# Optimization experiments

Hardware: AMD Instinct MI355X
Metric: run time of the kernel (lower is better)

## Reference

```python
import jax, jax.numpy as jnp
import numpy as np

B, C, L = 32, 64, 512
PATCH_LEN = 16
PATCH_NUM = L // PATCH_LEN
H = 512          # hidden_dim
FF = 512         # moe_d_ff == hidden_dim per __init__
E = 8            # num_experts
TOP_K = 2


def setup_inputs() -> dict:
    key = jax.random.key(0)
    ks = jax.random.split(key, 8)
    s = 0.02
    return {
        "x": jax.random.normal(ks[0], (B, C, L), dtype=jnp.float32),
        "Wp": jax.random.normal(ks[1], (H, PATCH_LEN), dtype=jnp.float32) * s,
        "bp": jnp.zeros((H,), dtype=jnp.float32),
        "Wg": jax.random.normal(ks[2], (E, H), dtype=jnp.float32) * s,
        "Wgate": jax.random.normal(ks[3], (E, FF, H), dtype=jnp.float32) * s,
        "Wup": jax.random.normal(ks[4], (E, FF, H), dtype=jnp.float32) * s,
        "Wdown": jax.random.normal(ks[5], (E, H, FF), dtype=jnp.float32) * s,
    }


def reference(x, Wp, bp, Wg, Wgate, Wup, Wdown):
    b, c, l = x.shape
    # patchify: [B, C, P, patch_len] -> project to hidden
    p = x.reshape(b, c, PATCH_NUM, PATCH_LEN)
    h = jnp.einsum("bcpl,dl->bcpd", p, Wp) + bp          # [B,C,P,H]
    tokens = h.reshape(-1, H)                               # [T,H]
    T = tokens.shape[0]

    # router: softmax in fp32, then top-k (norm_topk_prob=False)
    logits = tokens @ Wg.T                                   # [T,E]
    rw = jax.nn.softmax(logits.astype(jnp.float32), axis=-1)
    topw, topi = jax.lax.top_k(rw, TOP_K)                    # [T,K]

    # dense per-(token,expert) combine weight, equiv. to gather/scatter combine
    w = jnp.zeros((T, E), dtype=jnp.float32)
    w = w.at[jnp.arange(T)[:, None], topi].add(topw)         # [T,E]

    out = jnp.zeros((T, H), dtype=tokens.dtype)
    for e in range(E):  # fixed small expert loop
        g = jax.nn.silu(tokens @ Wgate[e].T)
        u = tokens @ Wup[e].T
        y = (g * u) @ Wdown[e].T                             # [T,H]
        out = out + (w[:, e:e + 1] * y.astype(jnp.float32)).astype(tokens.dtype)

    return out.reshape(b, c * PATCH_NUM, H)
```

## Files before the change

kernel.cpp:

```cpp
#include <hip/hip_runtime.h>
#include <hip/hip_bf16.h>
#include <cstdint>
#include <cstddef>

typedef __attribute__((ext_vector_type(8))) short short8;
typedef __attribute__((ext_vector_type(4))) float f32x4;

#define GLL16(g, l) __builtin_amdgcn_global_load_lds(                         \
    (const __attribute__((address_space(1))) void*)(g),                        \
    (__attribute__((address_space(3))) void*)(l), 16, 0, 0)

constexpr int kB = 32, kC = 64, kL = 512;
constexpr int kPL = 16, kPN = 32;
constexpr int kH = 512, kFF = 512, kE = 8;
constexpr int kT = kB * kC * kPN;
constexpr int kTilesPerSlot = 520;
constexpr int kMaxTiles = 2 * kTilesPerSlot;
constexpr int kMaxPairs = kMaxTiles * 128;

constexpr size_t OFF_TOK  = 0;
constexpr size_t OFF_GU   = OFF_TOK + (size_t)kT * kH * 2;
constexpr size_t OFF_TOPI = OFF_GU + (size_t)kMaxPairs * kFF * 2;
constexpr size_t OFF_TOPW = OFF_TOPI + (size_t)kT * 4;
constexpr size_t OFF_CCNT = OFF_TOPW + (size_t)kT * 8;
constexpr size_t OFF_COFF = OFF_CCNT + 256 * 16 * 4;
constexpr size_t OFF_EOFF = OFF_COFF + 256 * 16 * 4;
constexpr size_t OFF_TILE = OFF_EOFF + 256;
constexpr size_t OFF_PTOK = OFF_TILE + ((kMaxTiles * 4 + 255) & ~255ull);
constexpr size_t OFF_PW   = OFF_PTOK + (size_t)kMaxPairs * 4;
constexpr size_t OFF_DUMP = OFF_PW + (size_t)kMaxPairs * 4;
constexpr size_t OFF_BG   = OFF_DUMP + 128 * 512 * 4;
constexpr size_t OFF_BU   = OFF_BG + (size_t)kE * kFF * kH * 2;
constexpr size_t OFF_BD   = OFF_BU + (size_t)kE * kFF * kH * 2;
constexpr size_t OFF_WC   = OFF_BD + (size_t)kE * kH * kFF * 2;
constexpr size_t OFF_BC   = OFF_WC + 8 * 16 * 8;

__global__ __launch_bounds__(256) void k_conv3(const float* __restrict__ a,
                                               const float* __restrict__ b,
                                               const float* __restrict__ c,
                                               __hip_bfloat16* __restrict__ da,
                                               __hip_bfloat16* __restrict__ db,
                                               __hip_bfloat16* __restrict__ dc, int n) {
  for (int i = blockIdx.x * blockDim.x + threadIdx.x; i < 3 * n; i += gridDim.x * blockDim.x) {
    int reg = i / n, j = i - reg * n;
    const float* s = (reg == 0) ? a : (reg == 1) ? b : c;
    __hip_bfloat16* d = (reg == 0) ? da : (reg == 1) ? db : dc;
    d[j] = __float2bfloat16(s[j]);
  }
}

__global__ void k_wcomb(const float* __restrict__ Wg, const float* __restrict__ Wp,
                        const float* __restrict__ bp, double* __restrict__ wc,
                        double* __restrict__ bc) {
  int tid = threadIdx.x;
  int e = tid >> 4, l = tid & 15;
  double s = 0.0;
  for (int d = 0; d < kH; ++d) s += (double)Wg[e * kH + d] * (double)Wp[d * kPL + l];
  wc[e * kPL + l] = s;
  if (l == 0) {
    double b = 0.0;
    for (int d = 0; d < kH; ++d) b += (double)Wg[e * kH + d] * (double)bp[d];
    bc[e] = b;
  }
}

__global__ __launch_bounds__(256) void k_patch(const float* __restrict__ x,
                                               const float* __restrict__ Wp,
                                               const float* __restrict__ bp,
                                               __hip_bfloat16* __restrict__ tok) {
  __shared__ float sWp[512 * 17];
  __shared__ float sx[128];
  __shared__ float sbp[512];
  int bb = blockIdx.x;
  int bc = bb >> 2, pg = bb & 3;
  int tid = threadIdx.x;
  for (int i = tid; i < 512 * 16; i += 256) sWp[(i >> 4) * 17 + (i & 15)] = Wp[i];
  if (tid < 128) sx[tid] = x[(size_t)bc * 512 + pg * 128 + tid];
  for (int i = tid; i < 512; i += 256) sbp[i] = bp[i];
  __syncthreads();
  for (int tl = 0; tl < 8; ++tl) {
    int t = bc * kPN + pg * 8 + tl;
    const float* xp = &sx[tl * 16];
    for (int d = tid; d < 512; d += 256) {
      float s = sbp[d];
#pragma unroll
      for (int l = 0; l < 16; ++l) s += xp[l] * sWp[d * 17 + l];
      tok[(size_t)t * kH + d] = __float2bfloat16(s);
    }
  }
}

__global__ __launch_bounds__(256) void k_router(const float* __restrict__ x,
                                                const double* __restrict__ wc,
                                                const double* __restrict__ bc,
                                                int* __restrict__ topi,
                                                float* __restrict__ topw,
                                                int* __restrict__ chunkCnt) {
  int t = blockIdx.x * 256 + threadIdx.x;
  int bci = t >> 5, p = t & 31;
  const float* xp = &x[(size_t)bci * 512 + p * 16];
  double xl[16];
#pragma unroll
  for (int l = 0; l < 16; ++l) xl[l] = (double)xp[l];
  double lo[8];
  double m = -1e300;
#pragma unroll
  for (int e = 0; e < 8; ++e) {
    double s = bc[e];
#pragma unroll
    for (int l = 0; l < 16; ++l) s += xl[l] * wc[e * 16 + l];
    lo[e] = s;
    m = fmax(m, s);
  }
  double den = 0.0;
#pragma unroll
  for (int e = 0; e < 8; ++e) {
    lo[e] = exp(lo[e] - m);
    den += lo[e];
  }
  int i1 = 0;
  double v1 = lo[0];
#pragma unroll
  for (int e = 1; e < 8; ++e)
    if (lo[e] > v1) { v1 = lo[e]; i1 = e; }
  int i2 = -1;
  double v2 = -1.0;
#pragma unroll
  for (int e = 0; e < 8; ++e)
    if (e != i1 && lo[e] > v2) { v2 = lo[e]; i2 = e; }
  topi[t] = i1 | (i2 << 4);
  topw[2 * t] = (float)(v1 / den);
  topw[2 * t + 1] = (float)(v2 / den);

  __shared__ int wsum[16][4];
  int wave = threadIdx.x >> 6, lane = threadIdx.x & 63;
#pragma unroll
  for (int seg = 0; seg < 16; ++seg) {
    int e = seg & 7;
    bool sel = (seg < 8) ? (i1 == e) : (i2 == e);
    unsigned long long mm = __ballot(sel);
    if (lane == 0) wsum[seg][wave] = __popcll(mm);
  }
  __syncthreads();
  if (threadIdx.x < 16)
    chunkCnt[blockIdx.x * 16 + threadIdx.x] =
        wsum[threadIdx.x][0] + wsum[threadIdx.x][1] + wsum[threadIdx.x][2] + wsum[threadIdx.x][3];
}

__global__ __launch_bounds__(256) void k_scan(const int* __restrict__ chunkCnt,
                                              int* __restrict__ chunkOff,
                                              int* __restrict__ eoff,
                                              int* __restrict__ tileExpert,
                                              int* __restrict__ pairTok,
                                              float* __restrict__ pairW) {
  int tid = threadIdx.x;
  __shared__ int totals[16];
  __shared__ int base[16];
  __shared__ int padded[16];
  if (tid < 16) {
    int run = 0;
    for (int c = 0; c < 256; ++c) {
      chunkOff[c * 16 + tid] = run;
      run += chunkCnt[c * 16 + tid];
    }
    totals[tid] = run;
  }
  __syncthreads();
  if (tid == 0) {
    for (int s = 0; s < 2; ++s) {
      int b = s * kTilesPerSlot * 128;
      for (int e = 0; e < 8; ++e) {
        int seg = s * 8 + e;
        base[seg] = b;
        padded[seg] = (totals[seg] + 127) & ~127;
        b += padded[seg];
      }
    }
  }
  __syncthreads();
  if (tid < 16) eoff[tid] = base[tid];
  for (int tI = tid; tI < kMaxTiles; tI += 256) tileExpert[tI] = -1;
  __syncthreads();
  for (int seg = 0; seg < 16; ++seg) {
    int e = seg & 7;
    int tile0 = base[seg] >> 7, nt = padded[seg] >> 7;
    for (int tI = tid; tI < nt; tI += 256) tileExpert[tile0 + tI] = e;
    for (int p = base[seg] + totals[seg] + tid; p < base[seg] + padded[seg]; p += 256) {
      pairTok[p] = -1;
      pairW[p] = 0.f;
    }
  }
}

__global__ __launch_bounds__(256) void k_fill(const int* __restrict__ topi,
                                              const float* __restrict__ topw,
                                              const int* __restrict__ chunkOff,
                                              const int* __restrict__ eoff,
                                              int* __restrict__ pairTok,
                                              float* __restrict__ pairW) {
  int chunk = blockIdx.x;
  int t = chunk * 256 + threadIdx.x;
  int pk = topi[t];
  int i1 = pk & 15, i2 = (pk >> 4) & 15;
  float w1 = topw[2 * t], w2 = topw[2 * t + 1];
  int wave = threadIdx.x >> 6, lane = threadIdx.x & 63;
  __shared__ int wsum[16][4];
  int pre[16];
  bool sel[16];
#pragma unroll
  for (int seg = 0; seg < 16; ++seg) {
    int e = seg & 7;
    sel[seg] = (seg < 8) ? (i1 == e) : (i2 == e);
    unsigned long long mm = __ballot(sel[seg]);
    pre[seg] = __popcll(mm & ((1ull << lane) - 1));
    if (lane == 0) wsum[seg][wave] = __popcll(mm);
  }
  __syncthreads();
#pragma unroll
  for (int seg = 0; seg < 16; ++seg) {
    if (!sel[seg]) continue;
    int woff = 0;
    for (int w = 0; w < wave; ++w) woff += wsum[seg][w];
    int pos = eoff[seg] + chunkOff[chunk * 16 + seg] + woff + pre[seg];
    pairTok[pos] = t;
    pairW[pos] = (seg < 8) ? w1 : w2;
  }
}


__global__ __launch_bounds__(256, 2) void k_gateup_sp(const __hip_bfloat16* __restrict__ tok,
                                                      const __hip_bfloat16* __restrict__ Wg0,
                                                      const __hip_bfloat16* __restrict__ Wu0,
                                                      const int* __restrict__ pairTok,
                                                      const int* __restrict__ tileExpert,
                                                      __hip_bfloat16* __restrict__ GU) {
  const int e = tileExpert[blockIdx.x];
  if (e < 0) return;
  __shared__ __hip_bfloat16 As[128 * 32];
  __shared__ __hip_bfloat16 Bgs[128 * 32];
  __shared__ __hip_bfloat16 Bus[128 * 32];
  const int tid = threadIdx.x;
  const int wid = tid >> 6, lane = tid & 63;
  const int tileBase = blockIdx.x * 128, tileN = blockIdx.y * 128;
  const int wr = wid >> 1, wcol = wid & 1;
  const int r = lane & 15, kq = lane >> 4;

  f32x4 accg[4][4] = {};
  f32x4 accu[4][4] = {};

  const char* Ab = (const char*)tok;
  const char* Bgb = (const char*)(Wg0 + (size_t)e * kFF * kH);
  const char* Bub = (const char*)(Wu0 + (size_t)e * kFF * kH);
  const int off0 = wid * 1024 + lane * 16;
  const int row0 = off0 >> 6;
  const int col0 = ((((off0 >> 4) & 3) ^ ((row0 >> 1) & 3)) << 4);
  const int off1 = off0 + 4096;
  const int row1 = off1 >> 6;
  const int col1 = ((((off1 >> 4) & 3) ^ ((row1 >> 1) & 3)) << 4);
  int t0i = pairTok[tileBase + row0];
  int t1i = pairTok[tileBase + row1];
  const size_t t0 = (size_t)(t0i < 0 ? 0 : t0i);
  const size_t t1 = (size_t)(t1i < 0 ? 0 : t1i);

#pragma unroll 1
  for (int kt = 0; kt < 16; ++kt) {
    const int kb = kt * 64;
    GLL16(Ab + t0 * 1024 + kb + col0, (char*)As + wid * 1024);
    GLL16(Ab + t1 * 1024 + kb + col1, (char*)As + 4096 + wid * 1024);
    GLL16(Bgb + (size_t)(tileN + row0) * 1024 + kb + col0, (char*)Bgs + wid * 1024);
    GLL16(Bgb + (size_t)(tileN + row1) * 1024 + kb + col1, (char*)Bgs + 4096 + wid * 1024);
    GLL16(Bub + (size_t)(tileN + row0) * 1024 + kb + col0, (char*)Bus + wid * 1024);
    GLL16(Bub + (size_t)(tileN + row1) * 1024 + kb + col1, (char*)Bus + 4096 + wid * 1024);
    __syncthreads();

    short8 a[4], bg[4], bu[4];
#pragma unroll
    for (int i = 0; i < 4; ++i) {
      int row = wr * 64 + i * 16 + r;
      int sc = (kq ^ ((row >> 1) & 3)) << 3;
      a[i] = *(const short8*)&As[row * 32 + sc];
    }
#pragma unroll
    for (int j = 0; j < 4; ++j) {
      int row = wcol * 64 + j * 16 + r;
      int sc = (kq ^ ((row >> 1) & 3)) << 3;
      bg[j] = *(const short8*)&Bgs[row * 32 + sc];
      bu[j] = *(const short8*)&Bus[row * 32 + sc];
    }
#pragma unroll
    for (int i = 0; i < 4; ++i)
#pragma unroll
      for (int j = 0; j < 4; ++j) {
        accg[i][j] = __builtin_amdgcn_mfma_f32_16x16x32_bf16(a[i], bg[j], accg[i][j], 0, 0, 0);
        accu[i][j] = __builtin_amdgcn_mfma_f32_16x16x32_bf16(a[i], bu[j], accu[i][j], 0, 0, 0);
      }
    __syncthreads();
  }

#pragma unroll
  for (int i = 0; i < 4; ++i)
#pragma unroll
    for (int j = 0; j < 4; ++j)
#pragma unroll
      for (int q = 0; q < 4; ++q) {
        int row = tileBase + wr * 64 + i * 16 + kq * 4 + q;
        int col = tileN + wcol * 64 + j * 16 + r;
        float g = accg[i][j][q], u = accu[i][j][q];
        float val = g / (1.f + __expf(-g)) * u;
        GU[(size_t)row * kFF + col] = __float2bfloat16(val);
      }
}

__global__ __launch_bounds__(256, 2) void k_down_sp(const __hip_bfloat16* __restrict__ GU,
                                                    const __hip_bfloat16* __restrict__ Wd0,
                                                    const int* __restrict__ pairTok,
                                                    const float* __restrict__ pairW,
                                                    const int* __restrict__ tileExpert,
                                                    float* __restrict__ out,
                                                    float* __restrict__ dump,
                                                    int tileOff, int first) {
  const int tile = tileOff + blockIdx.x;
  const int e = tileExpert[tile];
  if (e < 0) return;
  __shared__ __hip_bfloat16 As[128 * 32];
  __shared__ __hip_bfloat16 Bs[128 * 32];
  const int tid = threadIdx.x;
  const int wid = tid >> 6, lane = tid & 63;
  const int tileBase = tile * 128, tileN = blockIdx.y * 128;
  const int wr = wid >> 1, wcol = wid & 1;
  const int r = lane & 15, kq = lane >> 4;

  f32x4 acc[4][4] = {};

  const char* Ab = (const char*)GU;
  const char* Bb = (const char*)(Wd0 + (size_t)e * kH * kFF);
  const int off0 = wid * 1024 + lane * 16;
  const int row0 = off0 >> 6;
  const int col0 = ((((off0 >> 4) & 3) ^ ((row0 >> 1) & 3)) << 4);
  const int off1 = off0 + 4096;
  const int row1 = off1 >> 6;
  const int col1 = ((((off1 >> 4) & 3) ^ ((row1 >> 1) & 3)) << 4);

#pragma unroll 1
  for (int kt = 0; kt < 16; ++kt) {
    const int kb = kt * 64;
    GLL16(Ab + (size_t)(tileBase + row0) * 1024 + kb + col0, (char*)As + wid * 1024);
    GLL16(Ab + (size_t)(tileBase + row1) * 1024 + kb + col1, (char*)As + 4096 + wid * 1024);
    GLL16(Bb + (size_t)(tileN + row0) * 1024 + kb + col0, (char*)Bs + wid * 1024);
    GLL16(Bb + (size_t)(tileN + row1) * 1024 + kb + col1, (char*)Bs + 4096 + wid * 1024);
    __syncthreads();

    short8 a[4], b[4];
#pragma unroll
    for (int i = 0; i < 4; ++i) {
      int row = wr * 64 + i * 16 + r;
      int sc = (kq ^ ((row >> 1) & 3)) << 3;
      a[i] = *(const short8*)&As[row * 32 + sc];
    }
#pragma unroll
    for (int j = 0; j < 4; ++j) {
      int row = wcol * 64 + j * 16 + r;
      int sc = (kq ^ ((row >> 1) & 3)) << 3;
      b[j] = *(const short8*)&Bs[row * 32 + sc];
    }
#pragma unroll
    for (int i = 0; i < 4; ++i)
#pragma unroll
      for (int j = 0; j < 4; ++j)
        acc[i][j] = __builtin_amdgcn_mfma_f32_16x16x32_bf16(a[i], b[j], acc[i][j], 0, 0, 0);
    __syncthreads();
  }

#pragma unroll
  for (int i = 0; i < 4; ++i)
#pragma unroll
    for (int q = 0; q < 4; ++q) {
      int prow = tileBase + wr * 64 + i * 16 + kq * 4 + q;
      float wv = pairW[prow];
      int tk = pairTok[prow];
      int colBase = tileN + wcol * 64 + r;
      float* orow = (tk >= 0) ? out + (size_t)tk * kH + colBase
                              : dump + (size_t)(prow & 127) * kH + colBase;
#pragma unroll
      for (int j = 0; j < 4; ++j) {
        float val = acc[i][j][q] * wv;
        if (first) orow[j * 16] = val;
        else orow[j * 16] += val;
      }
    }
}

extern "C" void kernel_launch(void* const* d_in, const int* in_sizes, int n_in,
                              void* d_out, int out_size, void* d_ws, size_t ws_size,
                              hipStream_t stream) {
  const float* x = (const float*)d_in[0];
  const float* Wp = (const float*)d_in[1];
  const float* bp = (const float*)d_in[2];
  const float* Wg = (const float*)d_in[3];
  const float* Wgate = (const float*)d_in[4];
  const float* Wup = (const float*)d_in[5];
  const float* Wdown = (const float*)d_in[6];
  float* out = (float*)d_out;

  char* ws = (char*)d_ws;
  __hip_bfloat16* tok = (__hip_bfloat16*)(ws + OFF_TOK);
  __hip_bfloat16* gu = (__hip_bfloat16*)(ws + OFF_GU);
  int* topi = (int*)(ws + OFF_TOPI);
  float* topw = (float*)(ws + OFF_TOPW);
  int* chunkCnt = (int*)(ws + OFF_CCNT);
  int* chunkOff = (int*)(ws + OFF_COFF);
  int* eoff = (int*)(ws + OFF_EOFF);
  int* tileExpert = (int*)(ws + OFF_TILE);
  int* pairTok = (int*)(ws + OFF_PTOK);
  float* pairW = (float*)(ws + OFF_PW);
  float* dump = (float*)(ws + OFF_DUMP);
  __hip_bfloat16* bgw = (__hip_bfloat16*)(ws + OFF_BG);
  __hip_bfloat16* buw = (__hip_bfloat16*)(ws + OFF_BU);
  __hip_bfloat16* bdw = (__hip_bfloat16*)(ws + OFF_BD);
  double* wc = (double*)(ws + OFF_WC);
  double* bcv = (double*)(ws + OFF_BC);

  const int nw = kE * kFF * kH;
  k_conv3<<<3072, 256, 0, stream>>>(Wgate, Wup, Wdown, bgw, buw, bdw, nw);
  k_wcomb<<<1, 128, 0, stream>>>(Wg, Wp, bp, wc, bcv);
  k_patch<<<8192, 256, 0, stream>>>(x, Wp, bp, tok);
  k_router<<<256, 256, 0, stream>>>(x, wc, bcv, topi, topw, chunkCnt);
  k_scan<<<1, 256, 0, stream>>>(chunkCnt, chunkOff, eoff, tileExpert, pairTok, pairW);
  k_fill<<<256, 256, 0, stream>>>(topi, topw, chunkOff, eoff, pairTok, pairW);

  dim3 gg(kMaxTiles, 4);
  k_gateup_sp<<<gg, 256, 0, stream>>>(tok, bgw, buw, pairTok, tileExpert, gu);
  dim3 gd(kTilesPerSlot, 4);
  k_down_sp<<<gd, 256, 0, stream>>>(gu, bdw, pairTok, pairW, tileExpert, out, dump, 0, 1);
  k_down_sp<<<gd, 256, 0, stream>>>(gu, bdw, pairTok, pairW, tileExpert, out, dump,
                                    kTilesPerSlot, 0);
}
```

Baseline: 542.3 us.

## Double-buffer LDS tiles in gate/up and down GEMMs; scan chunk counts in LDS

The gate/up and down expert GEMM kernels now use two LDS buffers. The next K-slice is issued with global_load_lds before the MFMAs on the current slice run, and the barrier at the end of each iteration waits for the prefetched data. This is meant to hide global load latency behind compute, at the cost of twice the LDS per block, which may lower occupancy. Separately, k_scan stages chunk counts and offsets in shared memory, so the serial per-segment prefix loop no longer reads and writes global memory directly.

```diff
diff --git a/kernel.cpp b/kernel.cpp
--- a/kernel.cpp
+++ b/kernel.cpp
@@ -154,18 +154,23 @@
                                               int* __restrict__ pairTok,
                                               float* __restrict__ pairW) {
   int tid = threadIdx.x;
+  __shared__ int cnt[256 * 16];
+  __shared__ int coff[256 * 16];
+  for (int i = tid; i < 256 * 16; i += 256) cnt[i] = chunkCnt[i];
+  __syncthreads();
   __shared__ int totals[16];
   __shared__ int base[16];
   __shared__ int padded[16];
   if (tid < 16) {
     int run = 0;
     for (int c = 0; c < 256; ++c) {
-      chunkOff[c * 16 + tid] = run;
-      run += chunkCnt[c * 16 + tid];
+      coff[c * 16 + tid] = run;
+      run += cnt[c * 16 + tid];
     }
     totals[tid] = run;
   }
   __syncthreads();
+  for (int i = tid; i < 256 * 16; i += 256) chunkOff[i] = coff[i];
   if (tid == 0) {
     for (int s = 0; s < 2; ++s) {
       int b = s * kTilesPerSlot * 128;
@@ -236,9 +241,9 @@
                                                       __hip_bfloat16* __restrict__ GU) {
   const int e = tileExpert[blockIdx.x];
   if (e < 0) return;
-  __shared__ __hip_bfloat16 As[128 * 32];
-  __shared__ __hip_bfloat16 Bgs[128 * 32];
-  __shared__ __hip_bfloat16 Bus[128 * 32];
+  __shared__ __hip_bfloat16 As[2][128 * 32];
+  __shared__ __hip_bfloat16 Bgs[2][128 * 32];
+  __shared__ __hip_bfloat16 Bus[2][128 * 32];
   const int tid = threadIdx.x;
   const int wid = tid >> 6, lane = tid & 63;
   const int tileBase = blockIdx.x * 128, tileN = blockIdx.y * 128;
@@ -262,30 +267,40 @@
   const size_t t0 = (size_t)(t0i < 0 ? 0 : t0i);
   const size_t t1 = (size_t)(t1i < 0 ? 0 : t1i);
 
-#pragma unroll 1
+  auto STAGE = [&](int buf, int kt) {
+    const int kb = kt * 64;
+    char* as = (char*)As[buf];
+    char* bgs = (char*)Bgs[buf];
+    char* bus = (char*)Bus[buf];
+    GLL16(Ab + t0 * 1024 + kb + col0, as + wid * 1024);
+    GLL16(Ab + t1 * 1024 + kb + col1, as + 4096 + wid * 1024);
+    GLL16(Bgb + (size_t)(tileN + row0) * 1024 + kb + col0, bgs + wid * 1024);
+    GLL16(Bgb + (size_t)(tileN + row1) * 1024 + kb + col1, bgs + 4096 + wid * 1024);
+    GLL16(Bub + (size_t)(tileN + row0) * 1024 + kb + col0, bus + wid * 1024);
+    GLL16(Bub + (size_t)(tileN + row1) * 1024 + kb + col1, bus + 4096 + wid * 1024);
+  };
+
+  STAGE(0, 0);
+  __syncthreads();
+
+#pragma unroll 2
   for (int kt = 0; kt < 16; ++kt) {
-    const int kb = kt * 64;
-    GLL16(Ab + t0 * 1024 + kb + col0, (char*)As + wid * 1024);
-    GLL16(Ab + t1 * 1024 + kb + col1, (char*)As + 4096 + wid * 1024);
-    GLL16(Bgb + (size_t)(tileN + row0) * 1024 + kb + col0, (char*)Bgs + wid * 1024);
-    GLL16(Bgb + (size_t)(tileN + row1) * 1024 + kb + col1, (char*)Bgs + 4096 + wid * 1024);
-    GLL16(Bub + (size_t)(tileN + row0) * 1024 + kb + col0, (char*)Bus + wid * 1024);
-    GLL16(Bub + (size_t)(tileN + row1) * 1024 + kb + col1, (char*)Bus + 4096 + wid * 1024);
-    __syncthreads();
+    const int cur = kt & 1;
+    if (kt < 15) STAGE(cur ^ 1, kt + 1);
 
     short8 a[4], bg[4], bu[4];
 #pragma unroll
     for (int i = 0; i < 4; ++i) {
       int row = wr * 64 + i * 16 + r;
       int sc = (kq ^ ((row >> 1) & 3)) << 3;
-      a[i] = *(const short8*)&As[row * 32 + sc];
+      a[i] = *(const short8*)&As[cur][row * 32 + sc];
     }
 #pragma unroll
     for (int j = 0; j < 4; ++j) {
       int row = wcol * 64 + j * 16 + r;
       int sc = (kq ^ ((row >> 1) & 3)) << 3;
-      bg[j] = *(const short8*)&Bgs[row * 32 + sc];
-      bu[j] = *(const short8*)&Bus[row * 32 + sc];
+      bg[j] = *(const short8*)&Bgs[cur][row * 32 + sc];
+      bu[j] = *(const short8*)&Bus[cur][row * 32 + sc];
     }
 #pragma unroll
     for (int i = 0; i < 4; ++i)
@@ -322,8 +337,8 @@
   const int tile = tileOff + blockIdx.x;
   const int e = tileExpert[tile];
   if (e < 0) return;
-  __shared__ __hip_bfloat16 As[128 * 32];
-  __shared__ __hip_bfloat16 Bs[128 * 32];
+  __shared__ __hip_bfloat16 As[2][128 * 32];
+  __shared__ __hip_bfloat16 Bs[2][128 * 32];
   const int tid = threadIdx.x;
   const int wid = tid >> 6, lane = tid & 63;
   const int tileBase = tile * 128, tileN = blockIdx.y * 128;
@@ -341,27 +356,36 @@
   const int row1 = off1 >> 6;
   const int col1 = ((((off1 >> 4) & 3) ^ ((row1 >> 1) & 3)) << 4);
 
-#pragma unroll 1
+  auto STAGE = [&](int buf, int kt) {
+    const int kb = kt * 64;
+    char* as = (char*)As[buf];
+    char* bs = (char*)Bs[buf];
+    GLL16(Ab + (size_t)(tileBase + row0) * 1024 + kb + col0, as + wid * 1024);
+    GLL16(Ab + (size_t)(tileBase + row1) * 1024 + kb + col1, as + 4096 + wid * 1024);
+    GLL16(Bb + (size_t)(tileN + row0) * 1024 + kb + col0, bs + wid * 1024);
+    GLL16(Bb + (size_t)(tileN + row1) * 1024 + kb + col1, bs + 4096 + wid * 1024);
+  };
+
+  STAGE(0, 0);
+  __syncthreads();
+
+#pragma unroll 2
   for (int kt = 0; kt < 16; ++kt) {
-    const int kb = kt * 64;
-    GLL16(Ab + (size_t)(tileBase + row0) * 1024 + kb + col0, (char*)As + wid * 1024);
-    GLL16(Ab + (size_t)(tileBase + row1) * 1024 + kb + col1, (char*)As + 4096 + wid * 1024);
-    GLL16(Bb + (size_t)(tileN + row0) * 1024 + kb + col0, (char*)Bs + wid * 1024);
-    GLL16(Bb + (size_t)(tileN + row1) * 1024 + kb + col1, (char*)Bs + 4096 + wid * 1024);
-    __syncthreads();
+    const int cur = kt & 1;
+    if (kt < 15) STAGE(cur ^ 1, kt + 1);
 
     short8 a[4], b[4];
 #pragma unroll
     for (int i = 0; i < 4; ++i) {
       int row = wr * 64 + i * 16 + r;
       int sc = (kq ^ ((row >> 1) & 3)) << 3;
-      a[i] = *(const short8*)&As[row * 32 + sc];
+      a[i] = *(const short8*)&As[cur][row * 32 + sc];
     }
 #pragma unroll
     for (int j = 0; j < 4; ++j) {
       int row = wcol * 64 + j * 16 + r;
       int sc = (kq ^ ((row >> 1) & 3)) << 3;
-      b[j] = *(const short8*)&Bs[row * 32 + sc];
+      b[j] = *(const short8*)&Bs[cur][row * 32 + sc];
     }
 #pragma unroll
     for (int i = 0; i < 4; ++i)
```

New measurement: 558.1 us. 1.03x slower.
